# Optimization experiments

Measured on AMD Instinct MI355X. Metric: run time of the kernel, lower is better.

The kernel has to match this reference:

```python
import jax, jax.numpy as jnp
import numpy as np

B, T, D, U = 64, 512, 256, 512


def setup_inputs() -> dict:
    key = jax.random.key(0)
    ks = jax.random.split(key, 8)
    g = lambda k, shape: (jax.random.normal(k, shape, dtype=jnp.float32) * 0.05)
    return {
        "x": jax.random.normal(ks[0], (B, T, D), dtype=jnp.float32),
        "h0": jnp.zeros((B, U), jnp.float32),
        "c0": jnp.zeros((B, U), jnp.float32),
        "W_f_short": g(ks[1], (D + U, U)),
        "b_f_short": -jnp.ones((U,), jnp.float32),
        "W_f_long": g(ks[2], (D + U, U)),
        "b_f_long": jnp.ones((U,), jnp.float32),
        "W_alpha": g(ks[3], (D + U, U)),
        "b_alpha": jnp.zeros((U,), jnp.float32),
        "W_m": g(ks[4], (D + U, D)),
        "b_m": jnp.zeros((D,), jnp.float32),
        "W_C": g(ks[5], (D + U, U)),
        "b_C": jnp.zeros((U,), jnp.float32),
        "W_o": g(ks[6], (D + U, U)),
        "b_o": jnp.zeros((U,), jnp.float32),
    }


def reference(x, h0, c0, W_f_short, b_f_short, W_f_long, b_f_long,
              W_alpha, b_alpha, W_m, b_m, W_C, b_C, W_o, b_o):
    # Fuse the five matmuls that share the same input hx=[h_prev, x_t]
    # into one; W_C uses a different input (hxm) and stays separate.
    units = h0.shape[-1]
    d = x.shape[-1]
    W_cat = jnp.concatenate([W_f_short, W_f_long, W_alpha, W_o, W_m], axis=1)
    b_cat = jnp.concatenate([b_f_short, b_f_long, b_alpha, b_o, b_m], axis=0)
    splits = np.cumsum([units, units, units, units])[:-0 or None]

    def step(carry, x_t):
        h_prev, c_prev = carry
        hx = jnp.concatenate([h_prev, x_t], axis=-1)          # [B, U+D]
        gates = hx @ W_cat + b_cat                            # [B, 4U+D]
        f_short = jax.nn.sigmoid(gates[:, :units])
        f_long = jax.nn.sigmoid(gates[:, units:2 * units])
        alpha = jax.nn.sigmoid(gates[:, 2 * units:3 * units])
        o_t = jax.nn.sigmoid(gates[:, 3 * units:4 * units])
        m_t = jax.nn.sigmoid(gates[:, 4 * units:])            # [B, D]
        f_t = alpha * f_short + (1.0 - alpha) * f_long
        i_t = 1.0 - f_t
        mod_x = m_t * x_t
        hxm = jnp.concatenate([h_prev, mod_x], axis=-1)
        c_hat = jnp.tanh(hxm @ W_C + b_C)
        c_t = f_t * c_prev + i_t * c_hat
        h_t = o_t * jnp.tanh(c_t)
        return (h_t, c_t), h_t

    xs = jnp.swapaxes(x, 0, 1)                                # [T, B, D]
    (_, _), hs = jax.lax.scan(step, (h0, c0), xs)             # hs: [T, B, U]
    return jnp.swapaxes(hs, 0, 1)                             # [B, T, U]
```

## Files before the change

kernel.cpp:

```cpp
#include <hip/hip_runtime.h>
#include <hip/hip_fp16.h>
#include <math.h>

typedef _Float16 h2 __attribute__((ext_vector_type(2)));
typedef _Float16 h8 __attribute__((ext_vector_type(8)));
typedef float    f4 __attribute__((ext_vector_type(4)));
typedef unsigned short     u16;
typedef unsigned int       u32;
typedef unsigned long long u64;

#define BB 64
#define TT 512
#define DD 256
#define UU 512

#define NBLK 64
#define CPB  44
#define XPB  36
#define UPB  8
#define MPB  4
#define NJ   2816
#define NJX  2304

#define OFF_W1   0ull
#define OFF_W2   (OFF_W1 + 2816ull*512*2)
#define OFF_WX   (OFF_W2 + 512ull*256*2)
#define OFF_B1   (OFF_WX + 2304ull*256*2)
#define OFF_HB   (OFF_B1 + 2816ull*4)
#define OFF_MX   (OFF_HB + 64ull*512*2)
#define OFF_CTR  (OFF_MX + 64ull*256*2)
#define OFF_XPRE (OFF_CTR + 16400ull*4)
#define WS_FULL  (OFF_XPRE + 512ull*2304*64*2)

__device__ __forceinline__ float sigf(float v)     { return 1.0f / (1.0f + __expf(-v)); }
__device__ __forceinline__ float tanhfast(float v) { return 1.0f - 2.0f / (__expf(2.0f * v) + 1.0f); }

__device__ __forceinline__ void plane_wait(u32* base, u32 tgt, int lane) {
    u32 it = 0;
    for (;;) {
        u32 v = __hip_atomic_load(base + lane * 16, __ATOMIC_RELAXED, __HIP_MEMORY_SCOPE_AGENT);
        if (__ballot(v >= tgt) == ~0ull) break;
        __builtin_amdgcn_s_sleep(1);
        if (++it > 4000000u) break;
    }
    (void)__hip_atomic_load(base + lane * 16, __ATOMIC_ACQUIRE, __HIP_MEMORY_SCOPE_AGENT);
}

__device__ __forceinline__ int pk5(int g, int u) { return (u >> 3) * 44 + g * 8 + (u & 7); }
__device__ __forceinline__ int pkm(int d)        { return (d >> 2) * 44 + 40 + (d & 3); }

__global__ void repack_kernel(const float* __restrict__ Wfs, const float* __restrict__ Wfl,
                              const float* __restrict__ Wal, const float* __restrict__ Wm,
                              const float* __restrict__ WC,  const float* __restrict__ Wo,
                              const float* __restrict__ bfs, const float* __restrict__ bfl,
                              const float* __restrict__ bal, const float* __restrict__ bm,
                              const float* __restrict__ bC,  const float* __restrict__ bo,
                              _Float16* __restrict__ W1, _Float16* __restrict__ W2,
                              _Float16* __restrict__ WxT, float* __restrict__ b1,
                              u32* __restrict__ ctr)
{
    const int stride = gridDim.x * blockDim.x;
    const int idx = blockIdx.x * blockDim.x + threadIdx.x;

    for (int i = idx; i < 2816 * 512; i += stride) {
        int J = i >> 9, k = i & 511;
        int blk = J / 44, c = J - blk * 44;
        float v;
        if (c < 40) {
            int grp = c >> 3, u = blk * 8 + (c & 7);
            const float* Wg = (grp == 0) ? Wfs : (grp == 1) ? Wfl : (grp == 2) ? Wal : (grp == 3) ? Wo : WC;
            v = Wg[(size_t)k * 512 + u];
        } else {
            int d = blk * 4 + (c - 40);
            v = Wm[(size_t)k * 256 + d];
        }
        W1[i] = (_Float16)v;
    }
    for (int i = idx; i < 512 * 256; i += stride) {
        int u = i >> 8, dd = i & 255;
        W2[i] = (_Float16)WC[(size_t)(512 + dd) * 512 + u];
    }
    for (int i = idx; i < 2304 * 256; i += stride) {
        int Jx = i >> 8, k2 = i & 255;
        int blk = Jx / 36, lc = Jx - blk * 36;
        float v;
        if (lc < 32) {
            int grp = lc >> 3, u = blk * 8 + (lc & 7);
            const float* Wg = (grp == 0) ? Wfs : (grp == 1) ? Wfl : (grp == 2) ? Wal : Wo;
            v = Wg[(size_t)(512 + k2) * 512 + u];
        } else {
            int d = blk * 4 + (lc - 32);
            v = Wm[(size_t)(512 + k2) * 256 + d];
        }
        WxT[i] = (_Float16)v;
    }
    for (int J = idx; J < 2816; J += stride) {
        int blk = J / 44, c = J - blk * 44;
        float v;
        if (c < 40) {
            int grp = c >> 3, u = blk * 8 + (c & 7);
            v = (grp == 0) ? bfs[u] : (grp == 1) ? bfl[u] : (grp == 2) ? bal[u] : (grp == 3) ? bo[u] : bC[u];
        } else {
            v = bm[blk * 4 + (c - 40)];
        }
        b1[J] = v;
    }
    for (int i = idx; i < 16400; i += stride) ctr[i] = 0;
}

__global__ __launch_bounds__(256) void xpre_kernel(const float* __restrict__ x,
                                                   const _Float16* __restrict__ WxT,
                                                   _Float16* __restrict__ Xpre)
{
    __shared__ _Float16 As[128 * 32];
    __shared__ _Float16 Bs[128 * 32];

    const int tid  = threadIdx.x;
    const int lane = tid & 63;
    const int w    = tid >> 6;
    const int wm   = w >> 1, wn = w & 1;
    const int quad = lane >> 4, l16 = lane & 15;
    const int row0 = blockIdx.x * 128;
    const int n0   = blockIdx.y * 128;

    f4 acc[4][4];
    for (int i = 0; i < 4; ++i)
        for (int j = 0; j < 4; ++j)
            acc[i][j] = (f4){0.f, 0.f, 0.f, 0.f};

    for (int kt = 0; kt < 8; ++kt) {
        const int k0 = kt * 32;
        {
            int r  = tid >> 3;
            int cg = (tid & 7) * 4;
            for (int rr = r; rr < 128; rr += 32) {
                f4 v = *(const f4*)&x[(size_t)(row0 + rr) * 256 + k0 + cg];
                As[rr * 32 + cg + 0] = (_Float16)v.x;
                As[rr * 32 + cg + 1] = (_Float16)v.y;
                As[rr * 32 + cg + 2] = (_Float16)v.z;
                As[rr * 32 + cg + 3] = (_Float16)v.w;
            }
        }
        {
            int r   = tid & 127;
            int seg = (tid >> 7) * 16;
            const _Float16* src = &WxT[(size_t)(n0 + r) * 256 + k0 + seg];
            *(f4*)&Bs[r * 32 + seg]     = *(const f4*)src;
            *(f4*)&Bs[r * 32 + seg + 8] = *(const f4*)(src + 8);
        }
        __syncthreads();

        h8 af[4], bfr[4];
#pragma unroll
        for (int f = 0; f < 4; ++f) {
            af[f]  = *(const h8*)&As[(wm * 64 + f * 16 + l16) * 32 + quad * 8];
            bfr[f] = *(const h8*)&Bs[(wn * 64 + f * 16 + l16) * 32 + quad * 8];
        }
#pragma unroll
        for (int fm = 0; fm < 4; ++fm)
#pragma unroll
            for (int fn = 0; fn < 4; ++fn)
                acc[fm][fn] = __builtin_amdgcn_mfma_f32_16x16x32_f16(af[fm], bfr[fn], acc[fm][fn], 0, 0, 0);
        __syncthreads();
    }

#pragma unroll
    for (int fm = 0; fm < 4; ++fm)
#pragma unroll
        for (int fn = 0; fn < 4; ++fn)
#pragma unroll
            for (int r = 0; r < 4; ++r) {
                int rr = row0 + wm * 64 + fm * 16 + quad * 4 + r;
                int J  = n0 + wn * 64 + fn * 16 + l16;
                int b = rr >> 9, tt = rr & 511;
                Xpre[((size_t)tt * NJX + J) * 64 + b] = (_Float16)acc[fm][fn][r];
            }
}

__global__ __launch_bounds__(256, 1) void rnn_coop(
    const float* __restrict__ x, const float* __restrict__ h0, const float* __restrict__ c0,
    const _Float16* __restrict__ W1, const _Float16* __restrict__ W2,
    const float* __restrict__ b1, const _Float16* __restrict__ Xpre,
    _Float16* __restrict__ hbuf, _Float16* __restrict__ mxbuf, u32* __restrict__ ctr,
    float* __restrict__ out)
{
    __shared__ __align__(16) _Float16 sW1[48 * 512];
    __shared__ float sB1[44];

    const int tid  = threadIdx.x;
    const int blk  = blockIdx.x;
    const int lane = tid & 63;
    const int q    = tid >> 6;
    const int l16  = lane & 15;
    const int quad = lane >> 4;
    const int swz  = l16 & 7;
    const int br   = q * 16 + l16;

    for (int idx = tid; idx < 48 * 64; idx += 256) {
        int r = idx >> 6, j = idx & 63;
        h8 v = {};
        if (r < CPB) v = *(const h8*)(W1 + ((size_t)(blk * CPB + r) * 512 + j * 8));
        *(h8*)&sW1[(r * 64 + (j ^ (r & 7))) * 8] = v;
    }
    h8 af2[8];
#pragma unroll
    for (int ks = 0; ks < 8; ++ks) {
        af2[ks] = (h8){};
        if (l16 < 8)
            af2[ks] = *(const h8*)(W2 + (size_t)(blk * UPB + l16) * 256 + ks * 32 + quad * 8);
    }
    if (tid < CPB) sB1[tid] = b1[blk * CPB + tid];
    float cr[4] = {0.f, 0.f, 0.f, 0.f};
    if (quad < 2) {
#pragma unroll
        for (int r = 0; r < 4; ++r)
            cr[r] = c0[(size_t)br * UU + blk * UPB + quad * 4 + r];
    }
    if (tid < 128) {
        int qq = tid >> 6, b = tid & 63;
        _Float16 hp[4];
#pragma unroll
        for (int r = 0; r < 4; ++r) hp[r] = (_Float16)h0[(size_t)b * UU + blk * UPB + qq * 4 + r];
        u64 hq; __builtin_memcpy(&hq, hp, 8);
        __hip_atomic_store((u64*)(hbuf + (size_t)b * 512 + blk * UPB + qq * 4), hq,
                           __ATOMIC_RELAXED, __HIP_MEMORY_SCOPE_AGENT);
    }
    __syncthreads();
    if (tid < 4)
        __hip_atomic_store(&ctr[(tid * 64 + blk) * 16], 1u,
                           __ATOMIC_RELAXED, __HIP_MEMORY_SCOPE_AGENT);

    u32* hfl = ctr + (size_t)q * 1024;
    u32* mfl = ctr + 4096 + (size_t)q * 1024;

    for (int t = 0; t < TT; ++t) {
        float pfs[4], pflv[4], pal[4], pov[4];
        float pxm[4] = {0.f, 0.f, 0.f, 0.f};
        f4 pxv = {0.f, 0.f, 0.f, 0.f};
        if (quad < 2) {
            const _Float16* xp = Xpre + ((size_t)t * NJX + blk * XPB) * 64 + br;
#pragma unroll
            for (int r = 0; r < 4; ++r) {
                int u = quad * 4 + r;
                pfs[r]  = (float)xp[(size_t)u * 64];
                pflv[r] = (float)xp[(size_t)(8 + u) * 64];
                pal[r]  = (float)xp[(size_t)(16 + u) * 64];
                pov[r]  = (float)xp[(size_t)(24 + u) * 64];
            }
        } else if (quad == 2) {
            const _Float16* xq = Xpre + ((size_t)t * NJX + blk * XPB + 32) * 64 + br;
#pragma unroll
            for (int r = 0; r < 4; ++r) pxm[r] = (float)xq[(size_t)r * 64];
            pxv = *(const f4*)&x[((size_t)br * TT + t) * DD + blk * MPB];
        }

        plane_wait(hfl, (u32)t + 1u, lane);

        h8 bf[16];
#pragma unroll
        for (int ks = 0; ks < 16; ++ks)
            bf[ks] = *(const h8*)(hbuf + (size_t)br * 512 + (ks * 4 + quad) * 8);

        f4 acc2 = {0.f, 0.f, 0.f, 0.f};
#pragma unroll
        for (int ks = 0; ks < 16; ++ks) {
            int jx = (ks * 4 + quad) ^ swz;
            h8 a2 = *(const h8*)&sW1[((32 + l16) * 64 + jx) * 8];
            acc2 = __builtin_amdgcn_mfma_f32_16x16x32_f16(a2, bf[ks], acc2, 0, 0, 0);
        }
        if (quad == 2) {
            _Float16 mp[4];
#pragma unroll
            for (int r = 0; r < 4; ++r) {
                float mr = acc2[r] + sB1[40 + r] + pxm[r];
                mp[r] = (_Float16)(sigf(mr) * pxv[r]);
            }
            u64 mq; __builtin_memcpy(&mq, mp, 8);
            __hip_atomic_store((u64*)(mxbuf + (size_t)br * 256 + blk * MPB), mq,
                               __ATOMIC_RELAXED, __HIP_MEMORY_SCOPE_AGENT);
        }

        f4 acc0 = {0.f, 0.f, 0.f, 0.f}, acc1 = {0.f, 0.f, 0.f, 0.f};
#pragma unroll
        for (int ks = 0; ks < 16; ++ks) {
            int jx = (ks * 4 + quad) ^ swz;
            h8 a0 = *(const h8*)&sW1[((     l16) * 64 + jx) * 8];
            h8 a1 = *(const h8*)&sW1[((16 + l16) * 64 + jx) * 8];
            acc0 = __builtin_amdgcn_mfma_f32_16x16x32_f16(a0, bf[ks], acc0, 0, 0, 0);
            acc1 = __builtin_amdgcn_mfma_f32_16x16x32_f16(a1, bf[ks], acc1, 0, 0, 0);
        }
        asm volatile("s_waitcnt vmcnt(0)" ::: "memory");
        if (quad == 2 && l16 == 0)
            __hip_atomic_store(&mfl[blk * 16], (u32)t + 1u,
                               __ATOMIC_RELAXED, __HIP_MEMORY_SCOPE_AGENT);

        float fv[4], ov[4], cpv[4];
#pragma unroll
        for (int r = 0; r < 4; ++r) {
            float flsh = __shfl_xor(acc0[r], 32);
            float osh  = __shfl_xor(acc1[r], 32);
            if (quad < 2) {
                int u = quad * 4 + r;
                float fs = sigf(acc0[r] + sB1[u]      + pfs[r]);
                float fl = sigf(flsh    + sB1[8 + u]  + pflv[r]);
                float al = sigf(acc1[r] + sB1[16 + u] + pal[r]);
                fv[r]  = al * fs + (1.0f - al) * fl;
                ov[r]  = sigf(osh + sB1[24 + u] + pov[r]);
                cpv[r] = acc2[r] + sB1[32 + u];
            }
        }

        plane_wait(mfl, (u32)t + 1u, lane);

        h8 bf2[8];
#pragma unroll
        for (int ks = 0; ks < 8; ++ks)
            bf2[ks] = *(const h8*)(mxbuf + (size_t)br * 256 + (ks * 4 + quad) * 8);
        f4 aq = {0.f, 0.f, 0.f, 0.f};
#pragma unroll
        for (int ks = 0; ks < 8; ++ks)
            aq = __builtin_amdgcn_mfma_f32_16x16x32_f16(af2[ks], bf2[ks], aq, 0, 0, 0);

        f4 ovec = {0.f, 0.f, 0.f, 0.f};
        if (quad < 2) {
            float hv[4];
#pragma unroll
            for (int r = 0; r < 4; ++r) {
                float ch = tanhfast(aq[r] + cpv[r]);
                float f  = fv[r];
                float c  = f * cr[r] + (1.0f - f) * ch;
                cr[r] = c;
                hv[r] = ov[r] * tanhfast(c);
            }
            _Float16 hp[4] = {(_Float16)hv[0], (_Float16)hv[1], (_Float16)hv[2], (_Float16)hv[3]};
            u64 hq; __builtin_memcpy(&hq, hp, 8);
            __hip_atomic_store((u64*)(hbuf + (size_t)br * 512 + blk * UPB + quad * 4), hq,
                               __ATOMIC_RELAXED, __HIP_MEMORY_SCOPE_AGENT);
            ovec = (f4){hv[0], hv[1], hv[2], hv[3]};
        }
        asm volatile("s_waitcnt vmcnt(0)" ::: "memory");
        if (lane == 0)
            __hip_atomic_store(&hfl[blk * 16], (u32)t + 2u,
                               __ATOMIC_RELAXED, __HIP_MEMORY_SCOPE_AGENT);
        if (quad < 2)
            __builtin_nontemporal_store(ovec,
                (f4*)&out[((size_t)br * TT + t) * UU + blk * UPB + quad * 4]);
    }
}

__global__ __launch_bounds__(704) void rnn_fb(const float* __restrict__ x,
                                              const float* __restrict__ h0,
                                              const float* __restrict__ c0,
                                              const _Float16* __restrict__ W1,
                                              const _Float16* __restrict__ W2,
                                              const _Float16* __restrict__ WxT,
                                              const float* __restrict__ b1g,
                                              float* __restrict__ out)
{
    __shared__ float g_ld[2816];
    __shared__ float b1_ld[2816];
    __shared__ float h_ld[512];
    __shared__ float x_ld[256];
    __shared__ float f_ld[512];
    __shared__ float o_ld[512];
    __shared__ float c_ld[512];
    __shared__ __align__(16) h2 hx_h2[256];
    __shared__ __align__(16) h2 x16_h2[128];
    __shared__ __align__(16) h2 modx_h2[128];

    const int tid = threadIdx.x;
    const int b   = blockIdx.x;
    const int j0  = tid * 4;
    const int c   = j0 % 44;
    const bool hasx = (c < 32) || (c >= 40);
    const int Jx0 = (j0 / 44) * 36 + (c < 32 ? c : c - 8);

    for (int j = tid; j < 2816; j += 704) b1_ld[j] = b1g[j];
    if (tid < 512) {
        h_ld[tid] = h0[b * 512 + tid];
        c_ld[tid] = c0[b * 512 + tid];
    }
    __syncthreads();

    const f4* __restrict__ w1r = (const f4*)(W1 + (size_t)j0 * 512);
    const float* __restrict__ xrow = x + (size_t)b * TT * DD;
    float* __restrict__ orow = out + (size_t)b * TT * UU;

    for (int t = 0; t < TT; ++t) {
        if (tid < 256) {
            h2 p; p[0] = (_Float16)h_ld[2 * tid]; p[1] = (_Float16)h_ld[2 * tid + 1];
            hx_h2[tid] = p;
        } else if (tid < 384) {
            int i = tid - 256;
            float v0 = xrow[t * DD + 2 * i];
            float v1 = xrow[t * DD + 2 * i + 1];
            x_ld[2 * i] = v0; x_ld[2 * i + 1] = v1;
            h2 p; p[0] = (_Float16)v0; p[1] = (_Float16)v1;
            x16_h2[i] = p;
        }
        __syncthreads();

        float a0 = b1_ld[j0], a1 = b1_ld[j0 + 1], a2 = b1_ld[j0 + 2], a3 = b1_ld[j0 + 3];
        if (hasx) {
            const f4* xr0 = (const f4*)(WxT + (size_t)Jx0 * 256);
            const f4* xr1 = xr0 + 32;
            const f4* xr2 = xr0 + 64;
            const f4* xr3 = xr0 + 96;
            const f4* xv4 = (const f4*)x16_h2;
#pragma unroll 4
            for (int kc = 0; kc < 32; ++kc) {
                f4 xv = xv4[kc];
                f4 w0 = xr0[kc], w1 = xr1[kc], w2 = xr2[kc], w3 = xr3[kc];
                const h2* xpv = (const h2*)&xv;
                const h2* p0 = (const h2*)&w0; const h2* p1 = (const h2*)&w1;
                const h2* p2 = (const h2*)&w2; const h2* p3 = (const h2*)&w3;
#pragma unroll
                for (int u = 0; u < 4; ++u) {
                    a0 = __builtin_amdgcn_fdot2(p0[u], xpv[u], a0, false);
                    a1 = __builtin_amdgcn_fdot2(p1[u], xpv[u], a1, false);
                    a2 = __builtin_amdgcn_fdot2(p2[u], xpv[u], a2, false);
                    a3 = __builtin_amdgcn_fdot2(p3[u], xpv[u], a3, false);
                }
            }
        }
        {
            const f4* hx4 = (const f4*)hx_h2;
            const f4* r0 = w1r;
            const f4* r1 = w1r + 64;
            const f4* r2 = w1r + 128;
            const f4* r3 = w1r + 192;
#pragma unroll 4
            for (int kc = 0; kc < 64; ++kc) {
                f4 hv = hx4[kc];
                f4 w0 = r0[kc], w1 = r1[kc], w2 = r2[kc], w3 = r3[kc];
                const h2* hp = (const h2*)&hv;
                const h2* p0 = (const h2*)&w0; const h2* p1 = (const h2*)&w1;
                const h2* p2 = (const h2*)&w2; const h2* p3 = (const h2*)&w3;
#pragma unroll
                for (int u = 0; u < 4; ++u) {
                    a0 = __builtin_amdgcn_fdot2(p0[u], hp[u], a0, false);
                    a1 = __builtin_amdgcn_fdot2(p1[u], hp[u], a1, false);
                    a2 = __builtin_amdgcn_fdot2(p2[u], hp[u], a2, false);
                    a3 = __builtin_amdgcn_fdot2(p3[u], hp[u], a3, false);
                }
            }
        }
        g_ld[j0] = a0; g_ld[j0 + 1] = a1; g_ld[j0 + 2] = a2; g_ld[j0 + 3] = a3;
        __syncthreads();

        if (tid < 128) {
            float m0 = sigf(g_ld[pkm(2 * tid)]);
            float m1 = sigf(g_ld[pkm(2 * tid + 1)]);
            h2 p;
            p[0] = (_Float16)(m0 * x_ld[2 * tid]);
            p[1] = (_Float16)(m1 * x_ld[2 * tid + 1]);
            modx_h2[tid] = p;
        } else if (tid < 640) {
            int u = tid - 128;
            float fs = sigf(g_ld[pk5(0, u)]);
            float fl = sigf(g_ld[pk5(1, u)]);
            float al = sigf(g_ld[pk5(2, u)]);
            f_ld[u] = al * fs + (1.0f - al) * fl;
            o_ld[u] = sigf(g_ld[pk5(3, u)]);
        }
        __syncthreads();

        if (tid < 512) {
            float s = g_ld[pk5(4, tid)];
            const f4* w2r = (const f4*)(W2 + (size_t)tid * 256);
            const f4* mx4 = (const f4*)modx_h2;
#pragma unroll 4
            for (int kc = 0; kc < 32; ++kc) {
                f4 wv = w2r[kc];
                f4 mv = mx4[kc];
                const h2* wp = (const h2*)&wv;
                const h2* mp = (const h2*)&mv;
#pragma unroll
                for (int u = 0; u < 4; ++u)
                    s = __builtin_amdgcn_fdot2(wp[u], mp[u], s, false);
            }
            float ch = tanhfast(s);
            float f  = f_ld[tid];
            float cc = f * c_ld[tid] + (1.0f - f) * ch;
            c_ld[tid] = cc;
            float h  = o_ld[tid] * tanhfast(cc);
            h_ld[tid] = h;
            orow[t * UU + tid] = h;
        }
        __syncthreads();
    }
}

extern "C" void kernel_launch(void* const* d_in, const int* in_sizes, int n_in,
                              void* d_out, int out_size, void* d_ws, size_t ws_size,
                              hipStream_t stream)
{
    (void)in_sizes; (void)n_in; (void)out_size;
    const float* x   = (const float*)d_in[0];
    const float* h0  = (const float*)d_in[1];
    const float* c0  = (const float*)d_in[2];
    const float* Wfs = (const float*)d_in[3];
    const float* bfs = (const float*)d_in[4];
    const float* Wfl = (const float*)d_in[5];
    const float* bfl = (const float*)d_in[6];
    const float* Wal = (const float*)d_in[7];
    const float* bal = (const float*)d_in[8];
    const float* Wm  = (const float*)d_in[9];
    const float* bm  = (const float*)d_in[10];
    const float* WC  = (const float*)d_in[11];
    const float* bC  = (const float*)d_in[12];
    const float* Wo  = (const float*)d_in[13];
    const float* bo  = (const float*)d_in[14];

    char* ws = (char*)d_ws;
    _Float16* W1   = (_Float16*)(ws + OFF_W1);
    _Float16* W2   = (_Float16*)(ws + OFF_W2);
    _Float16* WxT  = (_Float16*)(ws + OFF_WX);
    float*    b1   = (float*)   (ws + OFF_B1);
    _Float16* hbuf = (_Float16*)(ws + OFF_HB);
    _Float16* mxbf = (_Float16*)(ws + OFF_MX);
    u32*      ctr  = (u32*)     (ws + OFF_CTR);
    _Float16* Xpre = (_Float16*)(ws + OFF_XPRE);

    repack_kernel<<<dim3(1024), dim3(256), 0, stream>>>(
        Wfs, Wfl, Wal, Wm, WC, Wo, bfs, bfl, bal, bm, bC, bo, W1, W2, WxT, b1, ctr);

    if (ws_size >= WS_FULL) {
        xpre_kernel<<<dim3(256, 18), dim3(256), 0, stream>>>(x, WxT, Xpre);
        rnn_coop<<<dim3(NBLK), dim3(256), 0, stream>>>(
            x, h0, c0, W1, W2, b1, Xpre, hbuf, mxbf, ctr, (float*)d_out);
    } else {
        rnn_fb<<<dim3(BB), dim3(704), 0, stream>>>(
            x, h0, c0, W1, W2, WxT, b1, (float*)d_out);
    }
}
```

Before: 4.485 ms.

## Replace flag-counter barriers with tagged data records for inter-block sync

Removes the separate counter flags and the store-then-flag handshake (s_waitcnt plus flag store, then a spin on flags followed by a data load). Each pair of fp16 values is now packed with a timestep tag into a 64-bit atomic record, and consumers spin directly on the data until every tag matches. The goal is to cut one global round trip and the vmcnt drain from each of the two per-step synchronisation points. In exchange the h and m buffers double in size, each poll issues many more 64-bit atomic loads, and h0 initialisation moves into the repack kernel.

Result: faster. 4.055 ms (-9.6%).

```diff
diff --git a/kernel.cpp b/kernel.cpp
--- a/kernel.cpp
+++ b/kernel.cpp
@@ -27,23 +27,20 @@
 #define OFF_WX   (OFF_W2 + 512ull*256*2)
 #define OFF_B1   (OFF_WX + 2304ull*256*2)
 #define OFF_HB   (OFF_B1 + 2816ull*4)
-#define OFF_MX   (OFF_HB + 64ull*512*2)
-#define OFF_CTR  (OFF_MX + 64ull*256*2)
+#define OFF_MX   (OFF_HB + 256ull*64*8)
+#define OFF_CTR  (OFF_MX + 128ull*64*8)
 #define OFF_XPRE (OFF_CTR + 16400ull*4)
 #define WS_FULL  (OFF_XPRE + 512ull*2304*64*2)
 
 __device__ __forceinline__ float sigf(float v)     { return 1.0f / (1.0f + __expf(-v)); }
 __device__ __forceinline__ float tanhfast(float v) { return 1.0f - 2.0f / (__expf(2.0f * v) + 1.0f); }
 
-__device__ __forceinline__ void plane_wait(u32* base, u32 tgt, int lane) {
-    u32 it = 0;
-    for (;;) {
-        u32 v = __hip_atomic_load(base + lane * 16, __ATOMIC_RELAXED, __HIP_MEMORY_SCOPE_AGENT);
-        if (__ballot(v >= tgt) == ~0ull) break;
-        __builtin_amdgcn_s_sleep(1);
-        if (++it > 4000000u) break;
-    }
-    (void)__hip_atomic_load(base + lane * 16, __ATOMIC_ACQUIRE, __HIP_MEMORY_SCOPE_AGENT);
+__device__ __forceinline__ u64 pack_rec(float a, float b, u32 tag) {
+    _Float16 ha = (_Float16)a, hb = (_Float16)b;
+    u16 ua, ub;
+    __builtin_memcpy(&ua, &ha, 2);
+    __builtin_memcpy(&ub, &hb, 2);
+    return (u64)((u32)ua | ((u32)ub << 16)) | ((u64)tag << 32);
 }
 
 __device__ __forceinline__ int pk5(int g, int u) { return (u >> 3) * 44 + g * 8 + (u & 7); }
@@ -55,9 +52,10 @@
                               const float* __restrict__ bfs, const float* __restrict__ bfl,
                               const float* __restrict__ bal, const float* __restrict__ bm,
                               const float* __restrict__ bC,  const float* __restrict__ bo,
+                              const float* __restrict__ h0,
                               _Float16* __restrict__ W1, _Float16* __restrict__ W2,
                               _Float16* __restrict__ WxT, float* __restrict__ b1,
-                              u32* __restrict__ ctr)
+                              u64* __restrict__ hrec, u64* __restrict__ mrec)
 {
     const int stride = gridDim.x * blockDim.x;
     const int idx = blockIdx.x * blockDim.x + threadIdx.x;
@@ -105,7 +103,13 @@
         }
         b1[J] = v;
     }
-    for (int i = idx; i < 16400; i += stride) ctr[i] = 0;
+    for (int i = idx; i < 256 * 64; i += stride) {
+        int j = i >> 6, b = i & 63;
+        float v0 = h0[(size_t)b * UU + 2 * j];
+        float v1 = h0[(size_t)b * UU + 2 * j + 1];
+        hrec[(size_t)j * 64 + b] = pack_rec(v0, v1, 1u);
+    }
+    for (int i = idx; i < 128 * 64; i += stride) mrec[i] = 0ull;
 }
 
 __global__ __launch_bounds__(256) void xpre_kernel(const float* __restrict__ x,
@@ -178,10 +182,10 @@
 }
 
 __global__ __launch_bounds__(256, 1) void rnn_coop(
-    const float* __restrict__ x, const float* __restrict__ h0, const float* __restrict__ c0,
+    const float* __restrict__ x, const float* __restrict__ c0,
     const _Float16* __restrict__ W1, const _Float16* __restrict__ W2,
     const float* __restrict__ b1, const _Float16* __restrict__ Xpre,
-    _Float16* __restrict__ hbuf, _Float16* __restrict__ mxbuf, u32* __restrict__ ctr,
+    u64* __restrict__ hrec, u64* __restrict__ mrec,
     float* __restrict__ out)
 {
     __shared__ __align__(16) _Float16 sW1[48 * 512];
@@ -216,24 +220,11 @@
         for (int r = 0; r < 4; ++r)
             cr[r] = c0[(size_t)br * UU + blk * UPB + quad * 4 + r];
     }
-    if (tid < 128) {
-        int qq = tid >> 6, b = tid & 63;
-        _Float16 hp[4];
-#pragma unroll
-        for (int r = 0; r < 4; ++r) hp[r] = (_Float16)h0[(size_t)b * UU + blk * UPB + qq * 4 + r];
-        u64 hq; __builtin_memcpy(&hq, hp, 8);
-        __hip_atomic_store((u64*)(hbuf + (size_t)b * 512 + blk * UPB + qq * 4), hq,
-                           __ATOMIC_RELAXED, __HIP_MEMORY_SCOPE_AGENT);
-    }
     __syncthreads();
-    if (tid < 4)
-        __hip_atomic_store(&ctr[(tid * 64 + blk) * 16], 1u,
-                           __ATOMIC_RELAXED, __HIP_MEMORY_SCOPE_AGENT);
-
-    u32* hfl = ctr + (size_t)q * 1024;
-    u32* mfl = ctr + 4096 + (size_t)q * 1024;
 
     for (int t = 0; t < TT; ++t) {
+        const u32 expt = (u32)t + 1u;
+
         float pfs[4], pflv[4], pal[4], pov[4];
         float pxm[4] = {0.f, 0.f, 0.f, 0.f};
         f4 pxv = {0.f, 0.f, 0.f, 0.f};
@@ -254,12 +245,32 @@
             pxv = *(const f4*)&x[((size_t)br * TT + t) * DD + blk * MPB];
         }
 
-        plane_wait(hfl, (u32)t + 1u, lane);
-
         h8 bf[16];
-#pragma unroll
-        for (int ks = 0; ks < 16; ++ks)
-            bf[ks] = *(const h8*)(hbuf + (size_t)br * 512 + (ks * 4 + quad) * 8);
+        {
+            u32 guard = 0;
+            for (;;) {
+                u32 bad = 0;
+#pragma unroll
+                for (int ks = 0; ks < 16; ++ks) {
+                    const int j0 = (ks * 4 + quad) * 4;
+                    u64 r0 = __hip_atomic_load(hrec + (size_t)(j0 + 0) * 64 + br,
+                                               __ATOMIC_RELAXED, __HIP_MEMORY_SCOPE_AGENT);
+                    u64 r1 = __hip_atomic_load(hrec + (size_t)(j0 + 1) * 64 + br,
+                                               __ATOMIC_RELAXED, __HIP_MEMORY_SCOPE_AGENT);
+                    u64 r2 = __hip_atomic_load(hrec + (size_t)(j0 + 2) * 64 + br,
+                                               __ATOMIC_RELAXED, __HIP_MEMORY_SCOPE_AGENT);
+                    u64 r3 = __hip_atomic_load(hrec + (size_t)(j0 + 3) * 64 + br,
+                                               __ATOMIC_RELAXED, __HIP_MEMORY_SCOPE_AGENT);
+                    bad |= ((u32)(r0 >> 32) ^ expt) | ((u32)(r1 >> 32) ^ expt)
+                         | ((u32)(r2 >> 32) ^ expt) | ((u32)(r3 >> 32) ^ expt);
+                    u32 d[4] = {(u32)r0, (u32)r1, (u32)r2, (u32)r3};
+                    __builtin_memcpy(&bf[ks], d, 16);
+                }
+                if (__all(bad == 0)) break;
+                __builtin_amdgcn_s_sleep(2);
+                if (++guard > 1000000u) break;
+            }
+        }
 
         f4 acc2 = {0.f, 0.f, 0.f, 0.f};
 #pragma unroll
@@ -269,14 +280,13 @@
             acc2 = __builtin_amdgcn_mfma_f32_16x16x32_f16(a2, bf[ks], acc2, 0, 0, 0);
         }
         if (quad == 2) {
-            _Float16 mp[4];
-#pragma unroll
-            for (int r = 0; r < 4; ++r) {
-                float mr = acc2[r] + sB1[40 + r] + pxm[r];
-                mp[r] = (_Float16)(sigf(mr) * pxv[r]);
-            }
-            u64 mq; __builtin_memcpy(&mq, mp, 8);
-            __hip_atomic_store((u64*)(mxbuf + (size_t)br * 256 + blk * MPB), mq,
+            float m0 = sigf(acc2[0] + sB1[40] + pxm[0]) * pxv[0];
+            float m1 = sigf(acc2[1] + sB1[41] + pxm[1]) * pxv[1];
+            float m2 = sigf(acc2[2] + sB1[42] + pxm[2]) * pxv[2];
+            float m3 = sigf(acc2[3] + sB1[43] + pxm[3]) * pxv[3];
+            __hip_atomic_store(mrec + (size_t)(blk * 2 + 0) * 64 + br, pack_rec(m0, m1, expt),
+                               __ATOMIC_RELAXED, __HIP_MEMORY_SCOPE_AGENT);
+            __hip_atomic_store(mrec + (size_t)(blk * 2 + 1) * 64 + br, pack_rec(m2, m3, expt),
                                __ATOMIC_RELAXED, __HIP_MEMORY_SCOPE_AGENT);
         }
 
@@ -289,10 +299,6 @@
             acc0 = __builtin_amdgcn_mfma_f32_16x16x32_f16(a0, bf[ks], acc0, 0, 0, 0);
             acc1 = __builtin_amdgcn_mfma_f32_16x16x32_f16(a1, bf[ks], acc1, 0, 0, 0);
         }
-        asm volatile("s_waitcnt vmcnt(0)" ::: "memory");
-        if (quad == 2 && l16 == 0)
-            __hip_atomic_store(&mfl[blk * 16], (u32)t + 1u,
-                               __ATOMIC_RELAXED, __HIP_MEMORY_SCOPE_AGENT);
 
         float fv[4], ov[4], cpv[4];
 #pragma unroll
@@ -310,18 +316,38 @@
             }
         }
 
-        plane_wait(mfl, (u32)t + 1u, lane);
-
         h8 bf2[8];
-#pragma unroll
-        for (int ks = 0; ks < 8; ++ks)
-            bf2[ks] = *(const h8*)(mxbuf + (size_t)br * 256 + (ks * 4 + quad) * 8);
+        {
+            u32 guard = 0;
+            for (;;) {
+                u32 bad = 0;
+#pragma unroll
+                for (int ks = 0; ks < 8; ++ks) {
+                    const int j0 = (ks * 4 + quad) * 4;
+                    u64 r0 = __hip_atomic_load(mrec + (size_t)(j0 + 0) * 64 + br,
+                                               __ATOMIC_RELAXED, __HIP_MEMORY_SCOPE_AGENT);
+                    u64 r1 = __hip_atomic_load(mrec + (size_t)(j0 + 1) * 64 + br,
+                                               __ATOMIC_RELAXED, __HIP_MEMORY_SCOPE_AGENT);
+                    u64 r2 = __hip_atomic_load(mrec + (size_t)(j0 + 2) * 64 + br,
+                                               __ATOMIC_RELAXED, __HIP_MEMORY_SCOPE_AGENT);
+                    u64 r3 = __hip_atomic_load(mrec + (size_t)(j0 + 3) * 64 + br,
+                                               __ATOMIC_RELAXED, __HIP_MEMORY_SCOPE_AGENT);
+                    bad |= ((u32)(r0 >> 32) ^ expt) | ((u32)(r1 >> 32) ^ expt)
+                         | ((u32)(r2 >> 32) ^ expt) | ((u32)(r3 >> 32) ^ expt);
+                    u32 d[4] = {(u32)r0, (u32)r1, (u32)r2, (u32)r3};
+                    __builtin_memcpy(&bf2[ks], d, 16);
+                }
+                if (__all(bad == 0)) break;
+                __builtin_amdgcn_s_sleep(2);
+                if (++guard > 1000000u) break;
+            }
+        }
+
         f4 aq = {0.f, 0.f, 0.f, 0.f};
 #pragma unroll
         for (int ks = 0; ks < 8; ++ks)
             aq = __builtin_amdgcn_mfma_f32_16x16x32_f16(af2[ks], bf2[ks], aq, 0, 0, 0);
 
-        f4 ovec = {0.f, 0.f, 0.f, 0.f};
         if (quad < 2) {
             float hv[4];
 #pragma unroll
@@ -332,19 +358,16 @@
                 cr[r] = c;
                 hv[r] = ov[r] * tanhfast(c);
             }
-            _Float16 hp[4] = {(_Float16)hv[0], (_Float16)hv[1], (_Float16)hv[2], (_Float16)hv[3]};
-            u64 hq; __builtin_memcpy(&hq, hp, 8);
-            __hip_atomic_store((u64*)(hbuf + (size_t)br * 512 + blk * UPB + quad * 4), hq,
+            const u32 tagh = (u32)t + 2u;
+            const int j0 = blk * 4 + quad * 2;
+            __hip_atomic_store(hrec + (size_t)(j0 + 0) * 64 + br, pack_rec(hv[0], hv[1], tagh),
                                __ATOMIC_RELAXED, __HIP_MEMORY_SCOPE_AGENT);
-            ovec = (f4){hv[0], hv[1], hv[2], hv[3]};
-        }
-        asm volatile("s_waitcnt vmcnt(0)" ::: "memory");
-        if (lane == 0)
-            __hip_atomic_store(&hfl[blk * 16], (u32)t + 2u,
+            __hip_atomic_store(hrec + (size_t)(j0 + 1) * 64 + br, pack_rec(hv[2], hv[3], tagh),
                                __ATOMIC_RELAXED, __HIP_MEMORY_SCOPE_AGENT);
-        if (quad < 2)
+            f4 ovec = {hv[0], hv[1], hv[2], hv[3]};
             __builtin_nontemporal_store(ovec,
                 (f4*)&out[((size_t)br * TT + t) * UU + blk * UPB + quad * 4]);
+        }
     }
 }
 
@@ -517,18 +540,18 @@
     _Float16* W2   = (_Float16*)(ws + OFF_W2);
     _Float16* WxT  = (_Float16*)(ws + OFF_WX);
     float*    b1   = (float*)   (ws + OFF_B1);
-    _Float16* hbuf = (_Float16*)(ws + OFF_HB);
-    _Float16* mxbf = (_Float16*)(ws + OFF_MX);
-    u32*      ctr  = (u32*)     (ws + OFF_CTR);
+    u64*      hrec = (u64*)     (ws + OFF_HB);
+    u64*      mrec = (u64*)     (ws + OFF_MX);
     _Float16* Xpre = (_Float16*)(ws + OFF_XPRE);
 
     repack_kernel<<<dim3(1024), dim3(256), 0, stream>>>(
-        Wfs, Wfl, Wal, Wm, WC, Wo, bfs, bfl, bal, bm, bC, bo, W1, W2, WxT, b1, ctr);
+        Wfs, Wfl, Wal, Wm, WC, Wo, bfs, bfl, bal, bm, bC, bo, h0,
+        W1, W2, WxT, b1, hrec, mrec);
 
     if (ws_size >= WS_FULL) {
         xpre_kernel<<<dim3(256, 18), dim3(256), 0, stream>>>(x, WxT, Xpre);
         rnn_coop<<<dim3(NBLK), dim3(256), 0, stream>>>(
-            x, h0, c0, W1, W2, b1, Xpre, hbuf, mxbf, ctr, (float*)d_out);
+            x, c0, W1, W2, b1, Xpre, hrec, mrec, (float*)d_out);
     } else {
         rnn_fb<<<dim3(BB), dim3(704), 0, stream>>>(
             x, h0, c0, W1, W2, WxT, b1, (float*)d_out);
```
